# Kernel tuning notes

Hardware: AMD Instinct MI355X
Metric: run time of the kernel (lower is better)

Reference implementation:

```python
import jax, jax.numpy as jnp
import numpy as np

NEG_SLOPE = 0.2
BN_EPS = 1e-5
SM_EPS = 1e-16


def gatv2_conv(x, src, dst, num_nodes, Wl, bl, Wr, br, att, bias, concat):
    # x: [N, Fin]; att: [H, C]
    H, C = att.shape
    xl = (x @ Wl + bl).reshape(-1, H, C)  # source-side (x_j), lin_l
    xr = (x @ Wr + br).reshape(-1, H, C)  # target-side (x_i), lin_r
    e = jax.nn.leaky_relu(xl[src] + xr[dst], NEG_SLOPE)          # [E, H, C]
    logits = jnp.einsum('ehc,hc->eh', e, att)                    # [E, H]
    m = jax.ops.segment_max(logits, dst, num_segments=num_nodes)  # [N, H]
    expv = jnp.exp(logits - m[dst])
    denom = jax.ops.segment_sum(expv, dst, num_segments=num_nodes)
    alpha = expv / (denom[dst] + SM_EPS)                          # [E, H]
    msg = xl[src] * alpha[:, :, None]                             # [E, H, C]
    out = jax.ops.segment_sum(msg, dst, num_segments=num_nodes)   # [N, H, C]
    out = out.reshape(num_nodes, H * C) if concat else out.mean(axis=1)
    return out + bias


def batchnorm(x, gamma, beta):
    mean = x.mean(axis=0)
    var = x.var(axis=0)  # biased, as torch uses for normalization
    return gamma * (x - mean) * jax.lax.rsqrt(var + BN_EPS) + beta


def setup_inputs() -> dict:
    key = jax.random.key(0)
    ks = jax.random.split(key, 16)
    N, E = 50000, 800000
    Fin, Hid, Out, H = 128, 64, 64, 4
    s = 0.05
    inp = {
        'x': jax.random.normal(ks[0], (N, Fin), jnp.float32),
        'edge_index': jax.random.randint(ks[1], (2, E), 0, N, jnp.int64),
        # conv1 (heads=4, concat=False)
        'Wl1': jax.random.normal(ks[2], (Fin, H * Hid), jnp.float32) * s,
        'bl1': jnp.zeros((H * Hid,), jnp.float32),
        'Wr1': jax.random.normal(ks[3], (Fin, H * Hid), jnp.float32) * s,
        'br1': jnp.zeros((H * Hid,), jnp.float32),
        'att1': jax.random.normal(ks[4], (H, Hid), jnp.float32) * s,
        'bias1': jnp.zeros((Hid,), jnp.float32),
        'g1': jnp.ones((Hid,), jnp.float32),
        'beta1': jnp.zeros((Hid,), jnp.float32),
        # conv2 (heads=1, concat=True -> same as single head)
        'Wl2': jax.random.normal(ks[5], (Hid, Out), jnp.float32) * s,
        'bl2': jnp.zeros((Out,), jnp.float32),
        'Wr2': jax.random.normal(ks[6], (Hid, Out), jnp.float32) * s,
        'br2': jnp.zeros((Out,), jnp.float32),
        'att2': jax.random.normal(ks[7], (1, Out), jnp.float32) * s,
        'bias2': jnp.zeros((Out,), jnp.float32),
        'g2': jnp.ones((Out,), jnp.float32),
        'beta2': jnp.zeros((Out,), jnp.float32),
    }
    return inp


def reference(x, edge_index, Wl1, bl1, Wr1, br1, att1, bias1, g1, beta1,
              Wl2, bl2, Wr2, br2, att2, bias2, g2, beta2):
    N = x.shape[0]
    loops = jnp.arange(N, dtype=edge_index.dtype)  # PyG add_self_loops=True
    src = jnp.concatenate([edge_index[0], loops])
    dst = jnp.concatenate([edge_index[1], loops])
    h = gatv2_conv(x, src, dst, N, Wl1, bl1, Wr1, br1, att1, bias1, concat=False)
    h = jax.nn.relu(batchnorm(h, g1, beta1))  # dropout = identity (eval)
    h = gatv2_conv(h, src, dst, N, Wl2, bl2, Wr2, br2, att2, bias2, concat=True)
    h = jax.nn.relu(batchnorm(h, g2, beta2))
    return h
```

## Files before the change

kernel.cpp:

```cpp
#include <hip/hip_runtime.h>
#include <hip/hip_bf16.h>
#include <math.h>

#define TPB 256

typedef __attribute__((ext_vector_type(8))) short bfrag8;
typedef __attribute__((ext_vector_type(4))) float f32x4;

static __device__ __forceinline__ float bf2f(unsigned int u) {
  union { unsigned int i; float f; } c; c.i = u << 16; return c.f;
}
static __device__ __forceinline__ unsigned short f2bf(float f) {
  union { float f; unsigned int i; } c; c.f = f;
  unsigned int lsb = (c.i >> 16) & 1u;
  return (unsigned short)((c.i + 0x7fffu + lsb) >> 16);
}

#define DPP_ROR(v, C) __int_as_float(__builtin_amdgcn_update_dpp( \
    __float_as_int(v), __float_as_int(v), (C), 0xf, 0xf, false))
static __device__ __forceinline__ float red16(float p) {
  p += DPP_ROR(p, 0x121);
  p += DPP_ROR(p, 0x122);
  p += DPP_ROR(p, 0x124);
  p += DPP_ROR(p, 0x128);
  return p;
}

__global__ void k_deg_prep(const int* __restrict__ ei, int E, int ET, int* __restrict__ deg,
                           const float* __restrict__ Wl1, const float* __restrict__ Wr1,
                           const float* __restrict__ Wl2, const float* __restrict__ Wr2,
                           unsigned short* __restrict__ wt1l, unsigned short* __restrict__ wt1r,
                           unsigned short* __restrict__ wt2l, unsigned short* __restrict__ wt2r,
                           int egrid) {
  int b = blockIdx.x;
  if (b < egrid) {
    int e = b * TPB + threadIdx.x;
    if (e < ET) {
      int dst = (e < E) ? ei[E + e] : (e - E);
      atomicAdd(&deg[dst], 1);
    }
  } else {
    int i = (b - egrid) * TPB + threadIdx.x;
    if (i < 32768) {
      int c = i >> 7, k = i & 127;
      wt1l[i] = f2bf(Wl1[(size_t)k * 256 + c]);
    } else if (i < 65536) {
      int j = i - 32768; int c = j >> 7, k = j & 127;
      wt1r[j] = f2bf(Wr1[(size_t)k * 256 + c]);
    } else if (i < 69632) {
      int j = i - 65536; int c = j >> 6, k = j & 63;
      wt2l[j] = f2bf(Wl2[(size_t)k * 64 + c]);
    } else if (i < 73728) {
      int j = i - 69632; int c = j >> 6, k = j & 63;
      wt2r[j] = f2bf(Wr2[(size_t)k * 64 + c]);
    }
  }
}

__global__ void k_scan1(const int* __restrict__ deg, int N, int* __restrict__ bsum) {
  __shared__ int sm[TPB];
  int i = blockIdx.x * TPB + threadIdx.x;
  sm[threadIdx.x] = (i < N) ? ((deg[i] + 3) & ~3) : 0;
  __syncthreads();
  for (int d = TPB / 2; d > 0; d >>= 1) {
    if (threadIdx.x < d) sm[threadIdx.x] += sm[threadIdx.x + d];
    __syncthreads();
  }
  if (threadIdx.x == 0) bsum[blockIdx.x] = sm[0];
}

__global__ void k_scan3(const int* __restrict__ deg, const int* __restrict__ bsum,
                        int SB, int N, int* __restrict__ rowoff, int* __restrict__ cursor) {
  __shared__ int sm[TPB];
  int pv = (threadIdx.x < blockIdx.x) ? bsum[threadIdx.x] : 0;
  sm[threadIdx.x] = pv;
  __syncthreads();
  for (int dd = TPB / 2; dd > 0; dd >>= 1) {
    if (threadIdx.x < dd) sm[threadIdx.x] += sm[threadIdx.x + dd];
    __syncthreads();
  }
  int base = sm[0];
  __syncthreads();
  int i = blockIdx.x * TPB + threadIdx.x;
  int v = (i < N) ? ((deg[i] + 3) & ~3) : 0;
  sm[threadIdx.x] = v;
  __syncthreads();
  for (int dd = 1; dd < TPB; dd <<= 1) {
    int t = (threadIdx.x >= dd) ? sm[threadIdx.x - dd] : 0;
    __syncthreads();
    sm[threadIdx.x] += t;
    __syncthreads();
  }
  if (i < N) {
    int off = base + sm[threadIdx.x] - v;
    rowoff[i] = off;
    cursor[i] = off;
  }
}

__global__ void k_fill(const int* __restrict__ ei, int E, int ET,
                       int* __restrict__ cursor, int* __restrict__ csrc) {
  int e = blockIdx.x * blockDim.x + threadIdx.x;
  if (e >= ET) return;
  int src, dst;
  if (e < E) { src = ei[e]; dst = ei[E + e]; } else { src = dst = e - E; }
  int pos = atomicAdd(&cursor[dst], 1);
  csrc[pos] = src;
}

__global__ void k_gemm_mfma(const float* __restrict__ A, const float* __restrict__ affine,
                            const unsigned short* __restrict__ Wt0, const float* __restrict__ b0,
                            const unsigned short* __restrict__ Wt1, const float* __restrict__ b1,
                            unsigned short* __restrict__ out0, unsigned short* __restrict__ out1,
                            int M, int K, int Nc) {
  extern __shared__ short lds[];
  short* As = lds;
  short* Bls = lds + 64 * K;
  short* Brs = lds + 128 * K;
  const int r0 = blockIdx.x * 64;
  const int tid = threadIdx.x;
  const int Kb = K * 2;
  const int w = tid >> 6, lane = tid & 63;
  const int arow = w * 16 + (lane & 15);
  const int l16 = (lane >> 4) << 3;
  const int rbase0 = r0 + w * 16 + ((lane >> 4) << 2);

  const int fpr = K >> 2;
  for (int idx = tid; idx < 64 * fpr; idx += TPB) {
    int row = idx / fpr, c4 = idx - row * fpr;
    int gr = r0 + row;
    float4 v = make_float4(0.f, 0.f, 0.f, 0.f);
    if (gr < M) v = *(const float4*)(A + (size_t)gr * K + c4 * 4);
    if (affine) {
      int c = c4 * 4;
      v.x = fmaxf(v.x * affine[c + 0] + affine[64 + c + 0], 0.f);
      v.y = fmaxf(v.y * affine[c + 1] + affine[64 + c + 1], 0.f);
      v.z = fmaxf(v.z * affine[c + 2] + affine[64 + c + 2], 0.f);
      v.w = fmaxf(v.w * affine[c + 3] + affine[64 + c + 3], 0.f);
    }
    ushort4 pk; pk.x = f2bf(v.x); pk.y = f2bf(v.y); pk.z = f2bf(v.z); pk.w = f2bf(v.w);
    int kb = (c4 * 8) ^ ((row & 7) << 4);
    *(ushort4*)((char*)As + row * Kb + kb) = pk;
  }

  const int cpr = K >> 3;
  for (int nt = 0; nt < Nc; nt += 64) {
    __syncthreads();
    for (int idx = tid; idx < 64 * cpr; idx += TPB) {
      int c = idx / cpr, k8 = (idx - c * cpr) * 8;
      int kb = (k8 * 2) ^ ((c & 7) << 4);
      uint4 w0 = *(const uint4*)(Wt0 + (size_t)(nt + c) * K + k8);
      *(uint4*)((char*)Bls + c * Kb + kb) = w0;
      uint4 w1 = *(const uint4*)(Wt1 + (size_t)(nt + c) * K + k8);
      *(uint4*)((char*)Brs + c * Kb + kb) = w1;
    }
    __syncthreads();

    f32x4 accL[4], accR[4];
#pragma unroll
    for (int i = 0; i < 4; ++i) { accL[i] = (f32x4)0.f; accR[i] = (f32x4)0.f; }
    for (int k0 = 0; k0 < K; k0 += 32) {
      int kb = (k0 + l16) * 2;
      bfrag8 af = *(bfrag8*)((char*)As + arow * Kb + (kb ^ ((arow & 7) << 4)));
#pragma unroll
      for (int cf = 0; cf < 4; ++cf) {
        int col = cf * 16 + (lane & 15);
        int cb = col * Kb + (kb ^ ((col & 7) << 4));
        bfrag8 bl = *(bfrag8*)((char*)Bls + cb);
        accL[cf] = __builtin_amdgcn_mfma_f32_16x16x32_bf16(af, bl, accL[cf], 0, 0, 0);
        bfrag8 br = *(bfrag8*)((char*)Brs + cb);
        accR[cf] = __builtin_amdgcn_mfma_f32_16x16x32_bf16(af, br, accR[cf], 0, 0, 0);
      }
    }
    const int cbase = nt + (lane & 15);
#pragma unroll
    for (int cf = 0; cf < 4; ++cf) {
      int gcol = cbase + cf * 16;
      float bb0 = b0[gcol], bb1 = b1[gcol];
#pragma unroll
      for (int r = 0; r < 4; ++r) {
        int grow = rbase0 + r;
        if (grow < M) {
          out0[(size_t)grow * Nc + gcol] = f2bf(accL[cf][r] + bb0);
          out1[(size_t)grow * Nc + gcol] = f2bf(accR[cf][r] + bb1);
        }
      }
    }
  }
}

__global__ __launch_bounds__(TPB) void k_gat1(
    const unsigned short* __restrict__ xl, const unsigned short* __restrict__ xr,
    const int* __restrict__ rowoff, const int* __restrict__ deg,
    const int* __restrict__ csrc,
    const float* __restrict__ att, const float* __restrict__ bias,
    float* __restrict__ out, int N) {
  int node = (blockIdx.x * TPB + threadIdx.x) >> 6;
  int lane = threadIdx.x & 63;
  if (node >= N) return;
  int l4 = lane * 4;
  float4 atv = *(const float4*)(att + l4);
  float4 bb = *(const float4*)(bias + l4);
  uint2 rv = *(const uint2*)(xr + (node << 8) + l4);
  float xr0 = bf2f(rv.x & 0xffffu), xr1 = bf2f(rv.x >> 16);
  float xr2 = bf2f(rv.y & 0xffffu), xr3 = bf2f(rv.y >> 16);
  int beg = rowoff[node];
  int dg = deg[node];
  int endR = beg + dg;
  int endF = beg + (dg & ~3);
  float s = 0.f, a0 = 0.f, a1 = 0.f, a2 = 0.f, a3 = 0.f;
  int k = beg;
  for (; k < endF; k += 4) {
    int4 q = *(const int4*)(csrc + k);
    uint2 vv[4];
    vv[0] = *(const uint2*)(xl + (q.x << 8) + l4);
    vv[1] = *(const uint2*)(xl + (q.y << 8) + l4);
    vv[2] = *(const uint2*)(xl + (q.z << 8) + l4);
    vv[3] = *(const uint2*)(xl + (q.w << 8) + l4);
    float xs[4][4], ps[4];
#pragma unroll
    for (int u = 0; u < 4; ++u) {
      xs[u][0] = bf2f(vv[u].x & 0xffffu); xs[u][1] = bf2f(vv[u].x >> 16);
      xs[u][2] = bf2f(vv[u].y & 0xffffu); xs[u][3] = bf2f(vv[u].y >> 16);
      float t0 = xs[u][0] + xr0, t1 = xs[u][1] + xr1;
      float t2 = xs[u][2] + xr2, t3 = xs[u][3] + xr3;
      ps[u] = fmaxf(t0, 0.2f * t0) * atv.x + fmaxf(t1, 0.2f * t1) * atv.y
            + fmaxf(t2, 0.2f * t2) * atv.z + fmaxf(t3, 0.2f * t3) * atv.w;
    }
#pragma unroll
    for (int u = 0; u < 4; ++u) ps[u] = red16(ps[u]);
#pragma unroll
    for (int u = 0; u < 4; ++u) {
      float wv = __expf(ps[u]);
      s += wv;
      a0 += wv * xs[u][0]; a1 += wv * xs[u][1];
      a2 += wv * xs[u][2]; a3 += wv * xs[u][3];
    }
  }
  if (k < endR) {
    int4 q = *(const int4*)(csrc + k);
    uint2 vv[4];
    vv[0] = *(const uint2*)(xl + (q.x << 8) + l4);
    vv[1] = *(const uint2*)(xl + (q.y << 8) + l4);
    vv[2] = *(const uint2*)(xl + (q.z << 8) + l4);
    vv[3] = *(const uint2*)(xl + (q.w << 8) + l4);
    float xs[4][4], ps[4];
#pragma unroll
    for (int u = 0; u < 4; ++u) {
      xs[u][0] = bf2f(vv[u].x & 0xffffu); xs[u][1] = bf2f(vv[u].x >> 16);
      xs[u][2] = bf2f(vv[u].y & 0xffffu); xs[u][3] = bf2f(vv[u].y >> 16);
      float t0 = xs[u][0] + xr0, t1 = xs[u][1] + xr1;
      float t2 = xs[u][2] + xr2, t3 = xs[u][3] + xr3;
      ps[u] = fmaxf(t0, 0.2f * t0) * atv.x + fmaxf(t1, 0.2f * t1) * atv.y
            + fmaxf(t2, 0.2f * t2) * atv.z + fmaxf(t3, 0.2f * t3) * atv.w;
    }
#pragma unroll
    for (int u = 0; u < 4; ++u) ps[u] = red16(ps[u]);
#pragma unroll
    for (int u = 0; u < 4; ++u) {
      float wv = (k + u < endR) ? __expf(ps[u]) : 0.f;
      s += wv;
      a0 += wv * xs[u][0]; a1 += wv * xs[u][1];
      a2 += wv * xs[u][2]; a3 += wv * xs[u][3];
    }
  }
  float inv = 1.f / (s + 1e-16f);
  a0 *= inv; a1 *= inv; a2 *= inv; a3 *= inv;
  a0 += __shfl_xor(a0, 16); a0 += __shfl_xor(a0, 32);
  a1 += __shfl_xor(a1, 16); a1 += __shfl_xor(a1, 32);
  a2 += __shfl_xor(a2, 16); a2 += __shfl_xor(a2, 32);
  a3 += __shfl_xor(a3, 16); a3 += __shfl_xor(a3, 32);
  if (lane < 16) {
    float4 o;
    o.x = a0 * 0.25f + bb.x;
    o.y = a1 * 0.25f + bb.y;
    o.z = a2 * 0.25f + bb.z;
    o.w = a3 * 0.25f + bb.w;
    *(float4*)(out + (node << 6) + l4) = o;
  }
}

__global__ __launch_bounds__(TPB) void k_gat2(
    const unsigned short* __restrict__ xl, const unsigned short* __restrict__ xr,
    const int* __restrict__ rowoff, const int* __restrict__ deg,
    const int* __restrict__ csrc,
    const float* __restrict__ att, const float* __restrict__ bias,
    float* __restrict__ out, int N) {
  int node = (blockIdx.x * TPB + threadIdx.x) >> 6;
  int lane = threadIdx.x & 63;
  if (node >= N) return;
  int grp = lane >> 4, c4 = (lane & 15) * 4;
  float4 atv = *(const float4*)(att + c4);
  float4 bb = *(const float4*)(bias + c4);
  uint2 rv = *(const uint2*)(xr + (node << 6) + c4);
  float xr0 = bf2f(rv.x & 0xffffu), xr1 = bf2f(rv.x >> 16);
  float xr2 = bf2f(rv.y & 0xffffu), xr3 = bf2f(rv.y >> 16);
  int beg = rowoff[node];
  int dg = deg[node];
  int endR = beg + dg;
  int quads = (dg + 3) >> 2;
  float s = 0.f, a0 = 0.f, a1 = 0.f, a2 = 0.f, a3 = 0.f;
  for (int it = 0; it < quads; ++it) {
    int kk = beg + it * 4 + grp;
    int src = csrc[kk];
    bool ok = kk < endR;
    uint2 v = *(const uint2*)(xl + (src << 6) + c4);
    float x0 = bf2f(v.x & 0xffffu), x1 = bf2f(v.x >> 16);
    float x2 = bf2f(v.y & 0xffffu), x3 = bf2f(v.y >> 16);
    float t0 = x0 + xr0, t1 = x1 + xr1, t2 = x2 + xr2, t3 = x3 + xr3;
    float p = fmaxf(t0, 0.2f * t0) * atv.x + fmaxf(t1, 0.2f * t1) * atv.y
            + fmaxf(t2, 0.2f * t2) * atv.z + fmaxf(t3, 0.2f * t3) * atv.w;
    p = red16(p);
    float wv = ok ? __expf(p) : 0.f;
    s += wv;
    a0 += wv * x0; a1 += wv * x1; a2 += wv * x2; a3 += wv * x3;
  }
  s += __shfl_xor(s, 16); s += __shfl_xor(s, 32);
  a0 += __shfl_xor(a0, 16); a0 += __shfl_xor(a0, 32);
  a1 += __shfl_xor(a1, 16); a1 += __shfl_xor(a1, 32);
  a2 += __shfl_xor(a2, 16); a2 += __shfl_xor(a2, 32);
  a3 += __shfl_xor(a3, 16); a3 += __shfl_xor(a3, 32);
  if (lane < 16) {
    float inv = 1.f / (s + 1e-16f);
    float4 o;
    o.x = a0 * inv + bb.x;
    o.y = a1 * inv + bb.y;
    o.z = a2 * inv + bb.z;
    o.w = a3 * inv + bb.w;
    *(float4*)(out + (node << 6) + c4) = o;
  }
}

__global__ void k_bnstat(const float* __restrict__ in, int N, float* __restrict__ part) {
  __shared__ float sm[TPB], sq[TPB];
  int col = threadIdx.x & 63;
  int rq = threadIdx.x >> 6;
  float s = 0.f, q = 0.f;
  for (int r = blockIdx.x * 4 + rq; r < N; r += gridDim.x * 4) {
    float v = in[(size_t)r * 64 + col];
    s += v; q += v * v;
  }
  sm[threadIdx.x] = s; sq[threadIdx.x] = q;
  __syncthreads();
  if (threadIdx.x < 64) {
    s = sm[threadIdx.x] + sm[threadIdx.x + 64] + sm[threadIdx.x + 128] + sm[threadIdx.x + 192];
    q = sq[threadIdx.x] + sq[threadIdx.x + 64] + sq[threadIdx.x + 128] + sq[threadIdx.x + 192];
    part[(size_t)blockIdx.x * 128 + threadIdx.x] = s;
    part[(size_t)blockIdx.x * 128 + 64 + threadIdx.x] = q;
  }
}

__global__ void k_bnfin(const float* __restrict__ part, int B, int N,
                        const float* __restrict__ g, const float* __restrict__ beta,
                        float* __restrict__ ab) {
  int c = threadIdx.x;
  float s = 0.f, q = 0.f;
  for (int b = 0; b < B; ++b) {
    s += part[(size_t)b * 128 + c];
    q += part[(size_t)b * 128 + 64 + c];
  }
  float mean = s / (float)N;
  float var = q / (float)N - mean * mean;
  float a = g[c] * rsqrtf(var + 1e-5f);
  ab[c] = a;
  ab[64 + c] = beta[c] - mean * a;
}

__global__ void k_bnapply(const float* __restrict__ in, const float* __restrict__ ab,
                          float* __restrict__ out, int total4) {
  int idx = blockIdx.x * blockDim.x + threadIdx.x;
  if (idx >= total4) return;
  float4 v = *(const float4*)(in + (size_t)idx * 4);
  int c0 = (idx & 15) * 4;
  v.x = fmaxf(v.x * ab[c0 + 0] + ab[64 + c0 + 0], 0.f);
  v.y = fmaxf(v.y * ab[c0 + 1] + ab[64 + c0 + 1], 0.f);
  v.z = fmaxf(v.z * ab[c0 + 2] + ab[64 + c0 + 2], 0.f);
  v.w = fmaxf(v.w * ab[c0 + 3] + ab[64 + c0 + 3], 0.f);
  *(float4*)(out + (size_t)idx * 4) = v;
}

extern "C" void kernel_launch(void* const* d_in, const int* in_sizes, int n_in,
                              void* d_out, int out_size, void* d_ws, size_t ws_size,
                              hipStream_t stream) {
  const float* x     = (const float*)d_in[0];
  const int*   ei    = (const int*)d_in[1];
  const float* Wl1   = (const float*)d_in[2];
  const float* bl1   = (const float*)d_in[3];
  const float* Wr1   = (const float*)d_in[4];
  const float* br1   = (const float*)d_in[5];
  const float* att1  = (const float*)d_in[6];
  const float* bias1 = (const float*)d_in[7];
  const float* g1    = (const float*)d_in[8];
  const float* be1   = (const float*)d_in[9];
  const float* Wl2   = (const float*)d_in[10];
  const float* bl2   = (const float*)d_in[11];
  const float* Wr2   = (const float*)d_in[12];
  const float* br2   = (const float*)d_in[13];
  const float* att2  = (const float*)d_in[14];
  const float* bias2 = (const float*)d_in[15];
  const float* g2    = (const float*)d_in[16];
  const float* be2   = (const float*)d_in[17];
  float* out = (float*)d_out;

  const int N  = in_sizes[0] / 128;
  const int E  = in_sizes[1] / 2;
  const int ET = E + N;
  const int ETP = ET + 4 * ((N + 255) & ~255);
  const int SB = (N + TPB - 1) / TPB;

  char* p = (char*)d_ws;
  auto take = [&](size_t b) { char* q = p; p += (b + 255) & ~(size_t)255; return q; };

  unsigned short* xl1 = (unsigned short*)take((size_t)N * 256 * 2);
  unsigned short* xr1 = (unsigned short*)take((size_t)N * 256 * 2);
  unsigned short* xl2 = (unsigned short*)take((size_t)N * 64 * 2);
  unsigned short* xr2 = (unsigned short*)take((size_t)N * 64 * 2);
  float* out1 = (float*)take((size_t)N * 64 * 4);
  unsigned short* wt1l = (unsigned short*)take(256 * 128 * 2);
  unsigned short* wt1r = (unsigned short*)take(256 * 128 * 2);
  unsigned short* wt2l = (unsigned short*)take(64 * 64 * 2);
  unsigned short* wt2r = (unsigned short*)take(64 * 64 * 2);
  int* deg    = (int*)take((size_t)N * 4);
  int* csrc   = (int*)take((size_t)ETP * 4 + 16);
  size_t zero_bytes = (char*)(csrc + ETP) + 16 - (char*)deg;
  int* rowoff = (int*)take((size_t)(N + 1) * 4);
  int* cursor = (int*)take((size_t)N * 4);
  int* bsum   = (int*)take((size_t)SB * 4);
  float* part = (float*)take((size_t)256 * 128 * 4);
  float* ab1  = (float*)take(128 * 4);
  float* ab2  = (float*)take(128 * 4);
  (void)ws_size; (void)n_in; (void)out_size;

  int egrid = (ET + TPB - 1) / TPB;
  int wgrid = (73728 + TPB - 1) / TPB;
  int ngrid = (N + 3) / 4;
  int mtile = (N + 63) / 64;
  int total4 = N * 16;

  hipMemsetAsync(deg, 0, zero_bytes, stream);
  k_deg_prep<<<egrid + wgrid, TPB, 0, stream>>>(ei, E, ET, deg,
                                                Wl1, Wr1, Wl2, Wr2,
                                                wt1l, wt1r, wt2l, wt2r, egrid);
  k_scan1<<<SB, TPB, 0, stream>>>(deg, N, bsum);
  k_scan3<<<SB, TPB, 0, stream>>>(deg, bsum, SB, N, rowoff, cursor);
  k_fill<<<egrid, TPB, 0, stream>>>(ei, E, ET, cursor, csrc);

  k_gemm_mfma<<<mtile, TPB, 3 * 64 * 128 * 2, stream>>>(
      x, nullptr, wt1l, bl1, wt1r, br1, xl1, xr1, N, 128, 256);
  k_gat1<<<ngrid, TPB, 0, stream>>>(xl1, xr1, rowoff, deg, csrc, att1, bias1, out1, N);
  k_bnstat<<<256, TPB, 0, stream>>>(out1, N, part);
  k_bnfin<<<1, 64, 0, stream>>>(part, 256, N, g1, be1, ab1);

  k_gemm_mfma<<<mtile, TPB, 3 * 64 * 64 * 2, stream>>>(
      out1, ab1, wt2l, bl2, wt2r, br2, xl2, xr2, N, 64, 64);
  k_gat2<<<ngrid, TPB, 0, stream>>>(xl2, xr2, rowoff, deg, csrc, att2, bias2, out, N);
  k_bnstat<<<256, TPB, 0, stream>>>(out, N, part);
  k_bnfin<<<1, 64, 0, stream>>>(part, 256, N, g2, be2, ab2);
  k_bnapply<<<(total4 + TPB - 1) / TPB, TPB, 0, stream>>>(out, ab2, out, total4);
}
```

Baseline: 423.6 us.

## Switch intermediates to fp16, use packed-half attention math and 2D GEMM grid

Replaces bf16 storage and MFMA with fp16, and computes the GATv2 attention logits in the edge loops with packed half adds, max and fdot2 instead of scalar fp32 math. x is converted to fp16 in a fused prep kernel, and the BN1+ReLU affine moves into a separate kernel that writes fp16 input for the second GEMM. The GEMM now tiles output columns over a second grid dimension instead of looping inside the block, which gives more blocks. Doing the attention math in fp16 risks overflow and accuracy loss, and the extra conversion kernels add memory passes.

After: 414.0 us. 2.3% less time.

```diff
diff --git a/kernel.cpp b/kernel.cpp
--- a/kernel.cpp
+++ b/kernel.cpp
@@ -4,16 +4,15 @@
 
 #define TPB 256
 
-typedef __attribute__((ext_vector_type(8))) short bfrag8;
+typedef __attribute__((ext_vector_type(8))) _Float16 hfrag8;
+typedef __attribute__((ext_vector_type(2))) _Float16 h2;
 typedef __attribute__((ext_vector_type(4))) float f32x4;
 
-static __device__ __forceinline__ float bf2f(unsigned int u) {
-  union { unsigned int i; float f; } c; c.i = u << 16; return c.f;
-}
-static __device__ __forceinline__ unsigned short f2bf(float f) {
-  union { float f; unsigned int i; } c; c.f = f;
-  unsigned int lsb = (c.i >> 16) & 1u;
-  return (unsigned short)((c.i + 0x7fffu + lsb) >> 16);
+union HU { unsigned int u; h2 h; };
+
+static __device__ __forceinline__ h2 as_h2(unsigned int u) { HU c; c.u = u; return c.h; }
+static __device__ __forceinline__ unsigned short f2h_bits(float f) {
+  union { _Float16 h; unsigned short s; } c; c.h = (_Float16)f; return c.s;
 }
 
 #define DPP_ROR(v, C) __int_as_float(__builtin_amdgcn_update_dpp( \
@@ -26,34 +25,41 @@
   return p;
 }
 
-__global__ void k_deg_prep(const int* __restrict__ ei, int E, int ET, int* __restrict__ deg,
+__global__ void k_prep_all(const int* __restrict__ ei, int E, int ET, int* __restrict__ deg,
+                           const float* __restrict__ x,
                            const float* __restrict__ Wl1, const float* __restrict__ Wr1,
                            const float* __restrict__ Wl2, const float* __restrict__ Wr2,
+                           unsigned short* __restrict__ xb,
                            unsigned short* __restrict__ wt1l, unsigned short* __restrict__ wt1r,
                            unsigned short* __restrict__ wt2l, unsigned short* __restrict__ wt2r,
-                           int egrid) {
-  int b = blockIdx.x;
-  if (b < egrid) {
-    int e = b * TPB + threadIdx.x;
-    if (e < ET) {
-      int dst = (e < E) ? ei[E + e] : (e - E);
-      atomicAdd(&deg[dst], 1);
-    }
-  } else {
-    int i = (b - egrid) * TPB + threadIdx.x;
-    if (i < 32768) {
-      int c = i >> 7, k = i & 127;
-      wt1l[i] = f2bf(Wl1[(size_t)k * 256 + c]);
-    } else if (i < 65536) {
-      int j = i - 32768; int c = j >> 7, k = j & 127;
-      wt1r[j] = f2bf(Wr1[(size_t)k * 256 + c]);
-    } else if (i < 69632) {
-      int j = i - 65536; int c = j >> 6, k = j & 63;
-      wt2l[j] = f2bf(Wl2[(size_t)k * 64 + c]);
-    } else if (i < 73728) {
-      int j = i - 69632; int c = j >> 6, k = j & 63;
-      wt2r[j] = f2bf(Wr2[(size_t)k * 64 + c]);
-    }
+                           int nx4) {
+  int i = blockIdx.x * TPB + threadIdx.x;
+  if (i < ET) {
+    int dst = (i < E) ? ei[E + i] : (i - E);
+    atomicAdd(&deg[dst], 1);
+    return;
+  }
+  i -= ET;
+  if (i < nx4) {
+    float4 v = *(const float4*)(x + (size_t)i * 4);
+    ushort4 o;
+    o.x = f2h_bits(v.x); o.y = f2h_bits(v.y); o.z = f2h_bits(v.z); o.w = f2h_bits(v.w);
+    *(ushort4*)(xb + (size_t)i * 4) = o;
+    return;
+  }
+  i -= nx4;
+  if (i < 32768) {
+    int c = i >> 7, k = i & 127;
+    wt1l[i] = f2h_bits(Wl1[(size_t)k * 256 + c]);
+  } else if (i < 65536) {
+    int j = i - 32768; int c = j >> 7, k = j & 127;
+    wt1r[j] = f2h_bits(Wr1[(size_t)k * 256 + c]);
+  } else if (i < 69632) {
+    int j = i - 65536; int c = j >> 6, k = j & 63;
+    wt2l[j] = f2h_bits(Wl2[(size_t)k * 64 + c]);
+  } else if (i < 73728) {
+    int j = i - 69632; int c = j >> 6, k = j & 63;
+    wt2r[j] = f2h_bits(Wr2[(size_t)k * 64 + c]);
   }
 }
 
@@ -108,7 +114,7 @@
   csrc[pos] = src;
 }
 
-__global__ void k_gemm_mfma(const float* __restrict__ A, const float* __restrict__ affine,
+__global__ void k_gemm_mfma(const unsigned short* __restrict__ Ab,
                             const unsigned short* __restrict__ Wt0, const float* __restrict__ b0,
                             const unsigned short* __restrict__ Wt1, const float* __restrict__ b1,
                             unsigned short* __restrict__ out0, unsigned short* __restrict__ out1,
@@ -117,73 +123,56 @@
   short* As = lds;
   short* Bls = lds + 64 * K;
   short* Brs = lds + 128 * K;
-  const int r0 = blockIdx.x * 64;
+  const int r0 = blockIdx.x * 64, n0 = blockIdx.y * 64;
   const int tid = threadIdx.x;
   const int Kb = K * 2;
+  const int cpr = K >> 3;
+  const int chunks = 64 * cpr;
+  for (int idx = tid; idx < chunks; idx += TPB) {
+    int row = idx / cpr, k8 = (idx - row * cpr) * 8;
+    int kb = (k8 * 2) ^ ((row & 7) << 4);
+    int gr = r0 + row;
+    uint4 av = make_uint4(0, 0, 0, 0);
+    if (gr < M) av = *(const uint4*)(Ab + (size_t)gr * K + k8);
+    *(uint4*)((char*)As + row * Kb + kb) = av;
+    uint4 w0 = *(const uint4*)(Wt0 + (size_t)(n0 + row) * K + k8);
+    *(uint4*)((char*)Bls + row * Kb + kb) = w0;
+    uint4 w1 = *(const uint4*)(Wt1 + (size_t)(n0 + row) * K + k8);
+    *(uint4*)((char*)Brs + row * Kb + kb) = w1;
+  }
+  __syncthreads();
+
   const int w = tid >> 6, lane = tid & 63;
   const int arow = w * 16 + (lane & 15);
   const int l16 = (lane >> 4) << 3;
-  const int rbase0 = r0 + w * 16 + ((lane >> 4) << 2);
-
-  const int fpr = K >> 2;
-  for (int idx = tid; idx < 64 * fpr; idx += TPB) {
-    int row = idx / fpr, c4 = idx - row * fpr;
-    int gr = r0 + row;
-    float4 v = make_float4(0.f, 0.f, 0.f, 0.f);
-    if (gr < M) v = *(const float4*)(A + (size_t)gr * K + c4 * 4);
-    if (affine) {
-      int c = c4 * 4;
-      v.x = fmaxf(v.x * affine[c + 0] + affine[64 + c + 0], 0.f);
-      v.y = fmaxf(v.y * affine[c + 1] + affine[64 + c + 1], 0.f);
-      v.z = fmaxf(v.z * affine[c + 2] + affine[64 + c + 2], 0.f);
-      v.w = fmaxf(v.w * affine[c + 3] + affine[64 + c + 3], 0.f);
-    }
-    ushort4 pk; pk.x = f2bf(v.x); pk.y = f2bf(v.y); pk.z = f2bf(v.z); pk.w = f2bf(v.w);
-    int kb = (c4 * 8) ^ ((row & 7) << 4);
-    *(ushort4*)((char*)As + row * Kb + kb) = pk;
-  }
-
-  const int cpr = K >> 3;
-  for (int nt = 0; nt < Nc; nt += 64) {
-    __syncthreads();
-    for (int idx = tid; idx < 64 * cpr; idx += TPB) {
-      int c = idx / cpr, k8 = (idx - c * cpr) * 8;
-      int kb = (k8 * 2) ^ ((c & 7) << 4);
-      uint4 w0 = *(const uint4*)(Wt0 + (size_t)(nt + c) * K + k8);
-      *(uint4*)((char*)Bls + c * Kb + kb) = w0;
-      uint4 w1 = *(const uint4*)(Wt1 + (size_t)(nt + c) * K + k8);
-      *(uint4*)((char*)Brs + c * Kb + kb) = w1;
-    }
-    __syncthreads();
-
-    f32x4 accL[4], accR[4];
-#pragma unroll
-    for (int i = 0; i < 4; ++i) { accL[i] = (f32x4)0.f; accR[i] = (f32x4)0.f; }
-    for (int k0 = 0; k0 < K; k0 += 32) {
-      int kb = (k0 + l16) * 2;
-      bfrag8 af = *(bfrag8*)((char*)As + arow * Kb + (kb ^ ((arow & 7) << 4)));
-#pragma unroll
-      for (int cf = 0; cf < 4; ++cf) {
-        int col = cf * 16 + (lane & 15);
-        int cb = col * Kb + (kb ^ ((col & 7) << 4));
-        bfrag8 bl = *(bfrag8*)((char*)Bls + cb);
-        accL[cf] = __builtin_amdgcn_mfma_f32_16x16x32_bf16(af, bl, accL[cf], 0, 0, 0);
-        bfrag8 br = *(bfrag8*)((char*)Brs + cb);
-        accR[cf] = __builtin_amdgcn_mfma_f32_16x16x32_bf16(af, br, accR[cf], 0, 0, 0);
-      }
-    }
-    const int cbase = nt + (lane & 15);
+  f32x4 accL[4], accR[4];
+#pragma unroll
+  for (int i = 0; i < 4; ++i) { accL[i] = (f32x4)0.f; accR[i] = (f32x4)0.f; }
+  for (int k0 = 0; k0 < K; k0 += 32) {
+    int kb = (k0 + l16) * 2;
+    hfrag8 af = *(hfrag8*)((char*)As + arow * Kb + (kb ^ ((arow & 7) << 4)));
 #pragma unroll
     for (int cf = 0; cf < 4; ++cf) {
-      int gcol = cbase + cf * 16;
-      float bb0 = b0[gcol], bb1 = b1[gcol];
-#pragma unroll
-      for (int r = 0; r < 4; ++r) {
-        int grow = rbase0 + r;
-        if (grow < M) {
-          out0[(size_t)grow * Nc + gcol] = f2bf(accL[cf][r] + bb0);
-          out1[(size_t)grow * Nc + gcol] = f2bf(accR[cf][r] + bb1);
-        }
+      int col = cf * 16 + (lane & 15);
+      int cb = col * Kb + (kb ^ ((col & 7) << 4));
+      hfrag8 bl = *(hfrag8*)((char*)Bls + cb);
+      accL[cf] = __builtin_amdgcn_mfma_f32_16x16x32_f16(af, bl, accL[cf], 0, 0, 0);
+      hfrag8 br = *(hfrag8*)((char*)Brs + cb);
+      accR[cf] = __builtin_amdgcn_mfma_f32_16x16x32_f16(af, br, accR[cf], 0, 0, 0);
+    }
+  }
+  const int rbase = r0 + w * 16 + ((lane >> 4) << 2);
+  const int cbase = n0 + (lane & 15);
+#pragma unroll
+  for (int cf = 0; cf < 4; ++cf) {
+    int gcol = cbase + cf * 16;
+    float bb0 = b0[gcol], bb1 = b1[gcol];
+#pragma unroll
+    for (int r = 0; r < 4; ++r) {
+      int grow = rbase + r;
+      if (grow < M) {
+        out0[(size_t)grow * Nc + gcol] = f2h_bits(accL[cf][r] + bb0);
+        out1[(size_t)grow * Nc + gcol] = f2h_bits(accR[cf][r] + bb1);
       }
     }
   }
@@ -200,10 +189,13 @@
   if (node >= N) return;
   int l4 = lane * 4;
   float4 atv = *(const float4*)(att + l4);
+  h2 at01, at23;
+  at01.x = (_Float16)atv.x; at01.y = (_Float16)atv.y;
+  at23.x = (_Float16)atv.z; at23.y = (_Float16)atv.w;
   float4 bb = *(const float4*)(bias + l4);
   uint2 rv = *(const uint2*)(xr + (node << 8) + l4);
-  float xr0 = bf2f(rv.x & 0xffffu), xr1 = bf2f(rv.x >> 16);
-  float xr2 = bf2f(rv.y & 0xffffu), xr3 = bf2f(rv.y >> 16);
+  h2 xr01 = as_h2(rv.x), xr23 = as_h2(rv.y);
+  const _Float16 c02 = (_Float16)0.2f;
   int beg = rowoff[node];
   int dg = deg[node];
   int endR = beg + dg;
@@ -217,24 +209,25 @@
     vv[1] = *(const uint2*)(xl + (q.y << 8) + l4);
     vv[2] = *(const uint2*)(xl + (q.z << 8) + l4);
     vv[3] = *(const uint2*)(xl + (q.w << 8) + l4);
-    float xs[4][4], ps[4];
+    float ps[4];
 #pragma unroll
     for (int u = 0; u < 4; ++u) {
-      xs[u][0] = bf2f(vv[u].x & 0xffffu); xs[u][1] = bf2f(vv[u].x >> 16);
-      xs[u][2] = bf2f(vv[u].y & 0xffffu); xs[u][3] = bf2f(vv[u].y >> 16);
-      float t0 = xs[u][0] + xr0, t1 = xs[u][1] + xr1;
-      float t2 = xs[u][2] + xr2, t3 = xs[u][3] + xr3;
-      ps[u] = fmaxf(t0, 0.2f * t0) * atv.x + fmaxf(t1, 0.2f * t1) * atv.y
-            + fmaxf(t2, 0.2f * t2) * atv.z + fmaxf(t3, 0.2f * t3) * atv.w;
+      h2 x01 = as_h2(vv[u].x), x23 = as_h2(vv[u].y);
+      h2 t01 = x01 + xr01, t23 = x23 + xr23;
+      h2 l01 = __builtin_elementwise_max(t01, t01 * c02);
+      h2 l23 = __builtin_elementwise_max(t23, t23 * c02);
+      ps[u] = __builtin_amdgcn_fdot2(l01, at01,
+              __builtin_amdgcn_fdot2(l23, at23, 0.f, false), false);
     }
 #pragma unroll
     for (int u = 0; u < 4; ++u) ps[u] = red16(ps[u]);
 #pragma unroll
     for (int u = 0; u < 4; ++u) {
       float wv = __expf(ps[u]);
+      h2 x01 = as_h2(vv[u].x), x23 = as_h2(vv[u].y);
       s += wv;
-      a0 += wv * xs[u][0]; a1 += wv * xs[u][1];
-      a2 += wv * xs[u][2]; a3 += wv * xs[u][3];
+      a0 += wv * (float)x01.x; a1 += wv * (float)x01.y;
+      a2 += wv * (float)x23.x; a3 += wv * (float)x23.y;
     }
   }
   if (k < endR) {
@@ -244,24 +237,25 @@
     vv[1] = *(const uint2*)(xl + (q.y << 8) + l4);
     vv[2] = *(const uint2*)(xl + (q.z << 8) + l4);
     vv[3] = *(const uint2*)(xl + (q.w << 8) + l4);
-    float xs[4][4], ps[4];
+    float ps[4];
 #pragma unroll
     for (int u = 0; u < 4; ++u) {
-      xs[u][0] = bf2f(vv[u].x & 0xffffu); xs[u][1] = bf2f(vv[u].x >> 16);
-      xs[u][2] = bf2f(vv[u].y & 0xffffu); xs[u][3] = bf2f(vv[u].y >> 16);
-      float t0 = xs[u][0] + xr0, t1 = xs[u][1] + xr1;
-      float t2 = xs[u][2] + xr2, t3 = xs[u][3] + xr3;
-      ps[u] = fmaxf(t0, 0.2f * t0) * atv.x + fmaxf(t1, 0.2f * t1) * atv.y
-            + fmaxf(t2, 0.2f * t2) * atv.z + fmaxf(t3, 0.2f * t3) * atv.w;
+      h2 x01 = as_h2(vv[u].x), x23 = as_h2(vv[u].y);
+      h2 t01 = x01 + xr01, t23 = x23 + xr23;
+      h2 l01 = __builtin_elementwise_max(t01, t01 * c02);
+      h2 l23 = __builtin_elementwise_max(t23, t23 * c02);
+      ps[u] = __builtin_amdgcn_fdot2(l01, at01,
+              __builtin_amdgcn_fdot2(l23, at23, 0.f, false), false);
     }
 #pragma unroll
     for (int u = 0; u < 4; ++u) ps[u] = red16(ps[u]);
 #pragma unroll
     for (int u = 0; u < 4; ++u) {
       float wv = (k + u < endR) ? __expf(ps[u]) : 0.f;
+      h2 x01 = as_h2(vv[u].x), x23 = as_h2(vv[u].y);
       s += wv;
-      a0 += wv * xs[u][0]; a1 += wv * xs[u][1];
-      a2 += wv * xs[u][2]; a3 += wv * xs[u][3];
+      a0 += wv * (float)x01.x; a1 += wv * (float)x01.y;
+      a2 += wv * (float)x23.x; a3 += wv * (float)x23.y;
     }
   }
   float inv = 1.f / (s + 1e-16f);
@@ -291,10 +285,13 @@
   if (node >= N) return;
   int grp = lane >> 4, c4 = (lane & 15) * 4;
   float4 atv = *(const float4*)(att + c4);
+  h2 at01, at23;
+  at01.x = (_Float16)atv.x; at01.y = (_Float16)atv.y;
+  at23.x = (_Float16)atv.z; at23.y = (_Float16)atv.w;
   float4 bb = *(const float4*)(bias + c4);
   uint2 rv = *(const uint2*)(xr + (node << 6) + c4);
-  float xr0 = bf2f(rv.x & 0xffffu), xr1 = bf2f(rv.x >> 16);
-  float xr2 = bf2f(rv.y & 0xffffu), xr3 = bf2f(rv.y >> 16);
+  h2 xr01 = as_h2(rv.x), xr23 = as_h2(rv.y);
+  const _Float16 c02 = (_Float16)0.2f;
   int beg = rowoff[node];
   int dg = deg[node];
   int endR = beg + dg;
@@ -305,15 +302,17 @@
     int src = csrc[kk];
     bool ok = kk < endR;
     uint2 v = *(const uint2*)(xl + (src << 6) + c4);
-    float x0 = bf2f(v.x & 0xffffu), x1 = bf2f(v.x >> 16);
-    float x2 = bf2f(v.y & 0xffffu), x3 = bf2f(v.y >> 16);
-    float t0 = x0 + xr0, t1 = x1 + xr1, t2 = x2 + xr2, t3 = x3 + xr3;
-    float p = fmaxf(t0, 0.2f * t0) * atv.x + fmaxf(t1, 0.2f * t1) * atv.y
-            + fmaxf(t2, 0.2f * t2) * atv.z + fmaxf(t3, 0.2f * t3) * atv.w;
+    h2 x01 = as_h2(v.x), x23 = as_h2(v.y);
+    h2 t01 = x01 + xr01, t23 = x23 + xr23;
+    h2 l01 = __builtin_elementwise_max(t01, t01 * c02);
+    h2 l23 = __builtin_elementwise_max(t23, t23 * c02);
+    float p = __builtin_amdgcn_fdot2(l01, at01,
+              __builtin_amdgcn_fdot2(l23, at23, 0.f, false), false);
     p = red16(p);
     float wv = ok ? __expf(p) : 0.f;
     s += wv;
-    a0 += wv * x0; a1 += wv * x1; a2 += wv * x2; a3 += wv * x3;
+    a0 += wv * (float)x01.x; a1 += wv * (float)x01.y;
+    a2 += wv * (float)x23.x; a3 += wv * (float)x23.y;
   }
   s += __shfl_xor(s, 16); s += __shfl_xor(s, 32);
   a0 += __shfl_xor(a0, 16); a0 += __shfl_xor(a0, 32);
@@ -364,6 +363,20 @@
   float a = g[c] * rsqrtf(var + 1e-5f);
   ab[c] = a;
   ab[64 + c] = beta[c] - mean * a;
+}
+
+__global__ void k_prep2(const float* __restrict__ in, const float* __restrict__ ab,
+                        unsigned short* __restrict__ o, int n4) {
+  int i = blockIdx.x * blockDim.x + threadIdx.x;
+  if (i >= n4) return;
+  float4 v = *(const float4*)(in + (size_t)i * 4);
+  int c0 = (i & 15) * 4;
+  ushort4 u;
+  u.x = f2h_bits(fmaxf(v.x * ab[c0 + 0] + ab[64 + c0 + 0], 0.f));
+  u.y = f2h_bits(fmaxf(v.y * ab[c0 + 1] + ab[64 + c0 + 1], 0.f));
+  u.z = f2h_bits(fmaxf(v.z * ab[c0 + 2] + ab[64 + c0 + 2], 0.f));
+  u.w = f2h_bits(fmaxf(v.w * ab[c0 + 3] + ab[64 + c0 + 3], 0.f));
+  *(ushort4*)(o + (size_t)i * 4) = u;
 }
 
 __global__ void k_bnapply(const float* __restrict__ in, const float* __restrict__ ab,
@@ -416,6 +429,7 @@
   unsigned short* xl2 = (unsigned short*)take((size_t)N * 64 * 2);
   unsigned short* xr2 = (unsigned short*)take((size_t)N * 64 * 2);
   float* out1 = (float*)take((size_t)N * 64 * 4);
+  unsigned short* xb = (unsigned short*)take((size_t)N * 128 * 2);
   unsigned short* wt1l = (unsigned short*)take(256 * 128 * 2);
   unsigned short* wt1r = (unsigned short*)take(256 * 128 * 2);
   unsigned short* wt2l = (unsigned short*)take(64 * 64 * 2);
@@ -431,28 +445,31 @@
   float* ab2  = (float*)take(128 * 4);
   (void)ws_size; (void)n_in; (void)out_size;
 
+  unsigned short* A2 = xb;
+
   int egrid = (ET + TPB - 1) / TPB;
-  int wgrid = (73728 + TPB - 1) / TPB;
+  int nx4 = N * 32;
+  int ptot = ET + nx4 + 73728;
   int ngrid = (N + 3) / 4;
   int mtile = (N + 63) / 64;
   int total4 = N * 16;
 
   hipMemsetAsync(deg, 0, zero_bytes, stream);
-  k_deg_prep<<<egrid + wgrid, TPB, 0, stream>>>(ei, E, ET, deg,
-                                                Wl1, Wr1, Wl2, Wr2,
-                                                wt1l, wt1r, wt2l, wt2r, egrid);
+  k_prep_all<<<(ptot + TPB - 1) / TPB, TPB, 0, stream>>>(
+      ei, E, ET, deg, x, Wl1, Wr1, Wl2, Wr2, xb, wt1l, wt1r, wt2l, wt2r, nx4);
   k_scan1<<<SB, TPB, 0, stream>>>(deg, N, bsum);
   k_scan3<<<SB, TPB, 0, stream>>>(deg, bsum, SB, N, rowoff, cursor);
   k_fill<<<egrid, TPB, 0, stream>>>(ei, E, ET, cursor, csrc);
 
-  k_gemm_mfma<<<mtile, TPB, 3 * 64 * 128 * 2, stream>>>(
-      x, nullptr, wt1l, bl1, wt1r, br1, xl1, xr1, N, 128, 256);
+  k_gemm_mfma<<<dim3(mtile, 4), TPB, 3 * 64 * 128 * 2, stream>>>(
+      xb, wt1l, bl1, wt1r, br1, xl1, xr1, N, 128, 256);
   k_gat1<<<ngrid, TPB, 0, stream>>>(xl1, xr1, rowoff, deg, csrc, att1, bias1, out1, N);
   k_bnstat<<<256, TPB, 0, stream>>>(out1, N, part);
   k_bnfin<<<1, 64, 0, stream>>>(part, 256, N, g1, be1, ab1);
 
-  k_gemm_mfma<<<mtile, TPB, 3 * 64 * 64 * 2, stream>>>(
-      out1, ab1, wt2l, bl2, wt2r, br2, xl2, xr2, N, 64, 64);
+  k_prep2<<<(total4 + TPB - 1) / TPB, TPB, 0, stream>>>(out1, ab1, A2, total4);
+  k_gemm_mfma<<<dim3(mtile, 1), TPB, 3 * 64 * 64 * 2, stream>>>(
+      A2, wt2l, bl2, wt2r, br2, xl2, xr2, N, 64, 64);
   k_gat2<<<ngrid, TPB, 0, stream>>>(xl2, xr2, rowoff, deg, csrc, att2, bias2, out, N);
   k_bnstat<<<256, TPB, 0, stream>>>(out, N, part);
   k_bnfin<<<1, 64, 0, stream>>>(part, 256, N, g2, be2, ab2);
```
